# Optimization experiments

Measured on AMD Instinct MI355X. Metric: run time of the kernel, lower is better.

## Reference

```python
import jax, jax.numpy as jnp
import numpy as np

# Module config (matches init_kwargs)
ANCHORS = np.array([[4.0, 4.0, 4.0], [8.0, 8.0, 8.0], [16.0, 16.0, 16.0]], dtype=np.float32)  # (w,h,d) per anchor
NUM_CLASSES = 1
IMG_SIZE = (96, 96, 96)  # (W, H, D)

B, A = 16, 3
ATTRS = 5 + NUM_CLASSES
D = H = W = 48


def setup_inputs() -> dict:
    key = jax.random.key(0)
    inp = jax.random.normal(key, (B, A * ATTRS, D, H, W), dtype=jnp.float32)
    return {"inp": inp}


def reference(inp):
    b, _, d, h, w = inp.shape
    stride_w = IMG_SIZE[0] / w
    stride_h = IMG_SIZE[1] / h
    stride_d = IMG_SIZE[2] / d

    # [B, A, D, H, W, attrs]
    pred = inp.reshape(b, A, ATTRS, d, h, w).transpose(0, 1, 3, 4, 5, 2)

    x = jax.nn.sigmoid(pred[..., 0])
    y = jax.nn.sigmoid(pred[..., 1])
    z = jax.nn.sigmoid(pred[..., 2])
    l = pred[..., 3]
    conf = jax.nn.sigmoid(pred[..., 4])
    pred_cls = jax.nn.sigmoid(pred[..., 5:])

    # Broadcast grids (replaces the nested python-loop fills)
    grid_x = jnp.arange(w, dtype=inp.dtype)                    # (W,) -> last axis
    grid_y = jnp.arange(h, dtype=inp.dtype)[:, None]           # (H,1)
    grid_z = jnp.arange(d, dtype=inp.dtype)[:, None, None]     # (D,1,1)

    # Original uses scaled anchor WIDTH for the length channel
    anchor_len = (jnp.asarray(ANCHORS[:, 0], dtype=inp.dtype) / stride_w)[None, :, None, None, None]

    bx = (x + grid_x) * stride_w
    by = (y + grid_y) * stride_h
    bz = (z + grid_z) * stride_d
    bl = jnp.exp(l) * anchor_len * stride_w

    boxes = jnp.stack([bx, by, bz, bl], axis=-1)  # [B,A,D,H,W,4]

    out = jnp.concatenate(
        [boxes.reshape(b, -1, 4), conf.reshape(b, -1, 1), pred_cls.reshape(b, -1, NUM_CLASSES)],
        axis=-1,
    )
    return out
```

## Files before the change

kernel.cpp:

```cpp
#include <hip/hip_runtime.h>


#define DHW   110592
#define HW48  2304
#define SPB   1024
#define BPP   108
#define F4B   1536
#define F4P   165888
#define NBLK  5184

__device__ __forceinline__ float sigm(float v) {
    return 1.0f / (1.0f + __expf(-v));
}

__device__ __forceinline__ int swz(int i) {
    return (i & ~7) | ((i ^ (i >> 3)) & 7);
}

__global__ __launch_bounds__(256) void DecodeBox_kernel(
    const float* __restrict__ in, float* __restrict__ out) {
    __shared__ float4 lds[F4B];

    const int tid   = threadIdx.x;
    const int blk   = blockIdx.x;
    const int p     = blk / BPP;
    const int chunk = blk - p * BPP;
    const int a     = p % 3;

    const int S  = chunk * SPB + tid * 4;
    const int x0 = S % 48;
    const float yf = (float)((S / 48) % 48);
    const float zf = (float)(S / HW48);
    const float anchw = (a == 0) ? 4.0f : (a == 1) ? 8.0f : 16.0f;

    const float* ip = in + (size_t)p * (6 * DHW) + S;
    float4 tx = *(const float4*)(ip + 0 * DHW);
    float4 ty = *(const float4*)(ip + 1 * DHW);
    float4 tz = *(const float4*)(ip + 2 * DHW);
    float4 tl = *(const float4*)(ip + 3 * DHW);
    float4 tc = *(const float4*)(ip + 4 * DHW);
    float4 tk = *(const float4*)(ip + 5 * DHW);

    const float* txp = (const float*)&tx;
    const float* typ = (const float*)&ty;
    const float* tzp = (const float*)&tz;
    const float* tlp = (const float*)&tl;
    const float* tcp = (const float*)&tc;
    const float* tkp = (const float*)&tk;

    float bx[4], by[4], bz[4], bl[4], cf[4], cl[4];
#pragma unroll
    for (int q = 0; q < 4; ++q) {
        bx[q] = (sigm(txp[q]) + (float)(x0 + q)) * 2.0f;
        by[q] = (sigm(typ[q]) + yf) * 2.0f;
        bz[q] = (sigm(tzp[q]) + zf) * 2.0f;
        bl[q] = __expf(tlp[q]) * anchw;
        cf[q] = sigm(tcp[q]);
        cl[q] = sigm(tkp[q]);
    }

    const int wb = 6 * tid;
    lds[swz(wb + 0)] = make_float4(bx[0], by[0], bz[0], bl[0]);
    lds[swz(wb + 1)] = make_float4(cf[0], cl[0], bx[1], by[1]);
    lds[swz(wb + 2)] = make_float4(bz[1], bl[1], cf[1], cl[1]);
    lds[swz(wb + 3)] = make_float4(bx[2], by[2], bz[2], bl[2]);
    lds[swz(wb + 4)] = make_float4(cf[2], cl[2], bx[3], by[3]);
    lds[swz(wb + 5)] = make_float4(bz[3], bl[3], cf[3], cl[3]);

    __syncthreads();

    float4* op = (float4*)out + (size_t)p * F4P + (size_t)chunk * F4B;
#pragma unroll
    for (int k = 0; k < 6; ++k) {
        const int i = tid + 256 * k;
        op[i] = lds[swz(i)];
    }
}

extern "C" void kernel_launch(void* const* d_in, const int* in_sizes, int n_in,
                              void* d_out, int out_size, void* d_ws, size_t ws_size,
                              hipStream_t stream) {
    const float* in = (const float*)d_in[0];
    float* out = (float*)d_out;
    DecodeBox_kernel<<<NBLK, 256, 0, stream>>>(in, out);
}
```

Measured before the change: 220.3 us.

## Process two tiles per block with prefetched loads and nontemporal memory ops

```diff
diff --git a/kernel.cpp b/kernel.cpp
--- a/kernel.cpp
+++ b/kernel.cpp
@@ -1,13 +1,19 @@
 #include <hip/hip_runtime.h>
 
 
-#define DHW   110592
-#define HW48  2304
-#define SPB   1024
-#define BPP   108
-#define F4B   1536
-#define F4P   165888
-#define NBLK  5184
+typedef float vf4 __attribute__((ext_vector_type(4)));
+
+#define DHW    110592
+#define HW48   2304
+#define SPB    1024
+#define BPP    108
+#define F4B    1536
+#define F4P    165888
+#define CH4    27648
+#define TPB    2
+#define NBLK   2592
+
+struct Frag { vf4 x, y, z, l, c, k; };
 
 __device__ __forceinline__ float sigm(float v) {
     return 1.0f / (1.0f + __expf(-v));
@@ -17,63 +23,79 @@
     return (i & ~7) | ((i ^ (i >> 3)) & 7);
 }
 
-__global__ __launch_bounds__(256) void DecodeBox_kernel(
-    const float* __restrict__ in, float* __restrict__ out) {
-    __shared__ float4 lds[F4B];
+__device__ __forceinline__ void lds_barrier() {
+    asm volatile("s_waitcnt lgkmcnt(0)" ::: "memory");
+    __builtin_amdgcn_s_barrier();
+}
 
-    const int tid   = threadIdx.x;
-    const int blk   = blockIdx.x;
-    const int p     = blk / BPP;
-    const int chunk = blk - p * BPP;
-    const int a     = p % 3;
+__device__ __forceinline__ void load_frag(const float* __restrict__ in, int T,
+                                          int tid, Frag& f) {
+    const int p = T / BPP;
+    const int chunk = T - p * BPP;
+    const vf4* ip = (const vf4*)(in + (size_t)p * (6 * DHW) + chunk * SPB) + tid;
+    f.x = __builtin_nontemporal_load(ip + 0 * CH4);
+    f.y = __builtin_nontemporal_load(ip + 1 * CH4);
+    f.z = __builtin_nontemporal_load(ip + 2 * CH4);
+    f.l = __builtin_nontemporal_load(ip + 3 * CH4);
+    f.c = __builtin_nontemporal_load(ip + 4 * CH4);
+    f.k = __builtin_nontemporal_load(ip + 5 * CH4);
+}
 
-    const int S  = chunk * SPB + tid * 4;
-    const int x0 = S % 48;
+__device__ __forceinline__ void process(float* __restrict__ out, int T, int tid,
+                                        const Frag& f, vf4* lds) {
+    const int p = T / BPP;
+    const int chunk = T - p * BPP;
+    const int a = p % 3;
+    const float anchw = (a == 0) ? 4.0f : (a == 1) ? 8.0f : 16.0f;
+    const int S = chunk * SPB + tid * 4;
+    const float xf = (float)(S % 48);
     const float yf = (float)((S / 48) % 48);
     const float zf = (float)(S / HW48);
-    const float anchw = (a == 0) ? 4.0f : (a == 1) ? 8.0f : 16.0f;
-
-    const float* ip = in + (size_t)p * (6 * DHW) + S;
-    float4 tx = *(const float4*)(ip + 0 * DHW);
-    float4 ty = *(const float4*)(ip + 1 * DHW);
-    float4 tz = *(const float4*)(ip + 2 * DHW);
-    float4 tl = *(const float4*)(ip + 3 * DHW);
-    float4 tc = *(const float4*)(ip + 4 * DHW);
-    float4 tk = *(const float4*)(ip + 5 * DHW);
-
-    const float* txp = (const float*)&tx;
-    const float* typ = (const float*)&ty;
-    const float* tzp = (const float*)&tz;
-    const float* tlp = (const float*)&tl;
-    const float* tcp = (const float*)&tc;
-    const float* tkp = (const float*)&tk;
 
     float bx[4], by[4], bz[4], bl[4], cf[4], cl[4];
 #pragma unroll
     for (int q = 0; q < 4; ++q) {
-        bx[q] = (sigm(txp[q]) + (float)(x0 + q)) * 2.0f;
-        by[q] = (sigm(typ[q]) + yf) * 2.0f;
-        bz[q] = (sigm(tzp[q]) + zf) * 2.0f;
-        bl[q] = __expf(tlp[q]) * anchw;
-        cf[q] = sigm(tcp[q]);
-        cl[q] = sigm(tkp[q]);
+        bx[q] = (sigm(f.x[q]) + xf + (float)q) * 2.0f;
+        by[q] = (sigm(f.y[q]) + yf) * 2.0f;
+        bz[q] = (sigm(f.z[q]) + zf) * 2.0f;
+        bl[q] = __expf(f.l[q]) * anchw;
+        cf[q] = sigm(f.c[q]);
+        cl[q] = sigm(f.k[q]);
     }
 
     const int wb = 6 * tid;
-    lds[swz(wb + 0)] = make_float4(bx[0], by[0], bz[0], bl[0]);
-    lds[swz(wb + 1)] = make_float4(cf[0], cl[0], bx[1], by[1]);
-    lds[swz(wb + 2)] = make_float4(bz[1], bl[1], cf[1], cl[1]);
-    lds[swz(wb + 3)] = make_float4(bx[2], by[2], bz[2], bl[2]);
-    lds[swz(wb + 4)] = make_float4(cf[2], cl[2], bx[3], by[3]);
-    lds[swz(wb + 5)] = make_float4(bz[3], bl[3], cf[3], cl[3]);
+    lds[swz(wb + 0)] = (vf4){bx[0], by[0], bz[0], bl[0]};
+    lds[swz(wb + 1)] = (vf4){cf[0], cl[0], bx[1], by[1]};
+    lds[swz(wb + 2)] = (vf4){bz[1], bl[1], cf[1], cl[1]};
+    lds[swz(wb + 3)] = (vf4){bx[2], by[2], bz[2], bl[2]};
+    lds[swz(wb + 4)] = (vf4){cf[2], cl[2], bx[3], by[3]};
+    lds[swz(wb + 5)] = (vf4){bz[3], bl[3], cf[3], cl[3]};
 
-    __syncthreads();
+    lds_barrier();
 
-    float4* op = (float4*)out + (size_t)p * F4P + (size_t)chunk * F4B;
+    vf4* op = (vf4*)out + (size_t)p * F4P + (size_t)chunk * F4B;
 #pragma unroll
-    for (int k = 0; k < 6; ++k) {
-        const int i = tid + 256 * k;
-        op[i] = lds[swz(i)];
+    for (int kk = 0; kk < 6; ++kk) {
+        const int i = tid + 256 * kk;
+        __builtin_nontemporal_store(lds[swz(i)], op + i);
+    }
+
+    lds_barrier();
+}
+
+__global__ __launch_bounds__(256) void DecodeBox_kernel(
+    const float* __restrict__ in, float* __restrict__ out) {
+    __shared__ vf4 lds[F4B];
+    const int tid = threadIdx.x;
+    const int T0 = blockIdx.x * TPB;
+
+    Frag A, B;
+    load_frag(in, T0, tid, A);
+#pragma unroll
+    for (int t = 0; t < TPB; ++t) {
+        if (t + 1 < TPB) load_frag(in, T0 + t + 1, tid, B);
+        process(out, T0 + t, tid, A, lds);
+        A = B;
     }
 }
 
```

Measured after the change: 211.8 us. 1.04x faster.
